# Optimization experiments

Hardware: AMD Instinct MI355X
Metric: run time of the kernel (lower is better)

## Reference

```python
import jax, jax.numpy as jnp
import numpy as np

BATCH, SEQ, D_MODEL = 2, 2048, 1024
NUM_HEADS = 16
D_K = D_MODEL // NUM_HEADS  # 64
ROPE_THETA = 10000.0


def setup_inputs() -> dict:
    key = jax.random.key(0)
    ks = jax.random.split(key, 5)
    sigma = np.sqrt(2.0 / (D_MODEL + D_MODEL))
    return {
        "x": jax.random.normal(ks[0], (BATCH, SEQ, D_MODEL), dtype=jnp.float32),
        "Wq": jax.random.normal(ks[1], (D_MODEL, D_MODEL), dtype=jnp.float32) * sigma,
        "Wk": jax.random.normal(ks[2], (D_MODEL, D_MODEL), dtype=jnp.float32) * sigma,
        "Wv": jax.random.normal(ks[3], (D_MODEL, D_MODEL), dtype=jnp.float32) * sigma,
        "Wo": jax.random.normal(ks[4], (D_MODEL, D_MODEL), dtype=jnp.float32) * sigma,
        "token_positions": jnp.arange(SEQ, dtype=jnp.int32),
    }


def _rope(t, cos, sin):
    # t: [b, h, s, d_k]; cos/sin: [s, d_k//2]
    even, odd = t[..., ::2], t[..., 1::2]
    out_even = even * cos - odd * sin
    out_odd = odd * cos + even * sin
    return jnp.stack([out_even, out_odd], axis=-1).reshape(t.shape)


def reference(x, Wq, Wk, Wv, Wo, token_positions):
    b, s, d = x.shape
    h, dk = NUM_HEADS, D_K

    def split_heads(w):
        # Linear: einsum('... d_in, d_out d_in -> ... d_out')
        y = jnp.einsum('bsd,ed->bse', x, w)
        return y.reshape(b, s, h, dk).transpose(0, 2, 1, 3)  # [b,h,s,dk]

    q, k, v = split_heads(Wq), split_heads(Wk), split_heads(Wv)

    # RoPE tables from token positions
    inv_freq = 1.0 / (ROPE_THETA ** (jnp.arange(0, dk, 2, dtype=jnp.float32) / dk))
    freqs = token_positions.astype(jnp.float32)[:, None] * inv_freq[None, :]  # [s, dk/2]
    cos, sin = jnp.cos(freqs), jnp.sin(freqs)
    q = _rope(q, cos, sin)
    k = _rope(k, cos, sin)

    scale = 1.0 / jnp.sqrt(jnp.asarray(dk, dtype=x.dtype))
    scores = jnp.einsum('bhqd,bhkd->bhqk', q, k) * scale  # [b,h,s,s]
    causal = jnp.tril(jnp.ones((s, s), dtype=bool))
    scores = jnp.where(causal, scores, -jnp.inf)
    probs = jax.nn.softmax(scores, axis=-1)
    out = jnp.einsum('bhqk,bhkd->bhqd', probs, v)
    out = out.transpose(0, 2, 1, 3).reshape(b, s, d)
    return jnp.einsum('bsd,ed->bse', out, Wo)
```

## Files before the change

kernel.cpp:

```cpp
#include <hip/hip_runtime.h>
#include <hip/hip_bf16.h>


#define BATCH   2
#define SEQLEN  2048
#define DMODEL  1024
#define NHEADS  16
#define DK      64

typedef __attribute__((ext_vector_type(8))) short bf16x8;
typedef __attribute__((ext_vector_type(4))) short bf16x4;
typedef __attribute__((ext_vector_type(4))) float f32x4;

__device__ __forceinline__ float fast_exp2(float x) {
#if __has_builtin(__builtin_amdgcn_exp2f)
  return __builtin_amdgcn_exp2f(x);
#else
  return exp2f(x);
#endif
}

__device__ __forceinline__ bf16x8 load_cvt(const __hip_bfloat16* p) {
  return *(const bf16x8*)p;
}
__device__ __forceinline__ bf16x8 load_cvt(const float* p) {
  float4 a = *(const float4*)p;
  float4 b = *(const float4*)(p + 4);
  __hip_bfloat16 t[8];
  t[0] = __float2bfloat16(a.x); t[1] = __float2bfloat16(a.y);
  t[2] = __float2bfloat16(a.z); t[3] = __float2bfloat16(a.w);
  t[4] = __float2bfloat16(b.x); t[5] = __float2bfloat16(b.y);
  t[6] = __float2bfloat16(b.z); t[7] = __float2bfloat16(b.w);
  return *(const bf16x8*)t;
}

template <typename TA, typename TW>
__device__ __forceinline__ void gemm_core(
    const TA* __restrict__ A, const TW* __restrict__ W,
    int bm, int bn, int K, f32x4 (&acc)[4][4]) {
  __shared__ __hip_bfloat16 As[2][128 * 32];
  __shared__ __hip_bfloat16 Ws[2][128 * 32];
  const int tid  = threadIdx.x;
  const int wave = tid >> 6, lane = tid & 63;
  const int col  = lane & 15, quad = lane >> 4;
  const int wm   = (wave & 1) * 64, wn = (wave >> 1) * 64;
  const int srow = wave * 32;
  const int l4   = lane >> 2, sl = lane & 3;

  bf16x8 ra[2], rw[2];
  auto stage_load = [&](int k0) {
#pragma unroll
    for (int c = 0; c < 2; ++c) {
      int r = srow + c * 16 + l4;
      int g = sl ^ (r & 3);
      ra[c] = load_cvt(A + (size_t)(bm + r) * K + k0 + g * 8);
      rw[c] = load_cvt(W + (size_t)(bn + r) * K + k0 + g * 8);
    }
  };
  auto stage_write = [&](int buf) {
#pragma unroll
    for (int c = 0; c < 2; ++c) {
      int r = srow + c * 16 + l4;
      *(bf16x8*)&As[buf][r * 32 + sl * 8] = ra[c];
      *(bf16x8*)&Ws[buf][r * 32 + sl * 8] = rw[c];
    }
  };

  const int NK = K / 32;
  stage_load(0);
  stage_write(0);
  __syncthreads();

  for (int i = 0; i < NK; ++i) {
    const int buf = i & 1;
    const bool pre = (i + 1 < NK);
    if (pre) stage_load((i + 1) * 32);

    bf16x8 af[4], bfr[4];
#pragma unroll
    for (int mt = 0; mt < 4; ++mt) {
      int r = wm + mt * 16 + col;
      af[mt] = *(const bf16x8*)&As[buf][r * 32 + ((quad ^ (r & 3)) * 8)];
    }
#pragma unroll
    for (int nt = 0; nt < 4; ++nt) {
      int r = wn + nt * 16 + col;
      bfr[nt] = *(const bf16x8*)&Ws[buf][r * 32 + ((quad ^ (r & 3)) * 8)];
    }
#pragma unroll
    for (int mt = 0; mt < 4; ++mt)
#pragma unroll
      for (int nt = 0; nt < 4; ++nt)
        acc[mt][nt] = __builtin_amdgcn_mfma_f32_16x16x32_bf16(af[mt], bfr[nt], acc[mt][nt], 0, 0, 0);

    if (pre) stage_write(buf ^ 1);
    __syncthreads();
  }
}

__global__ __launch_bounds__(256) void mfma_qkv(
    const float* __restrict__ x,
    const float* __restrict__ wq,
    const float* __restrict__ wk,
    const float* __restrict__ wv,
    __hip_bfloat16* __restrict__ Qw,
    __hip_bfloat16* __restrict__ Kw,
    __hip_bfloat16* __restrict__ Vtw) {
  const int z = blockIdx.z;
  const float* W = (z == 0) ? wq : (z == 1) ? wk : wv;
  const int bm = blockIdx.x * 128, bn = blockIdx.y * 128;
  f32x4 acc[4][4] = {};
  gemm_core(x, W, bm, bn, DMODEL, acc);

  const int wave = threadIdx.x >> 6, lane = threadIdx.x & 63;
  const int col  = lane & 15, quad = lane >> 4;
  const int wm   = (wave & 1) * 64, wn = (wave >> 1) * 64;

  if (z < 2) {
    __hip_bfloat16* C = (z == 0) ? Qw : Kw;
#pragma unroll
    for (int mt = 0; mt < 4; ++mt)
#pragma unroll
      for (int nt = 0; nt < 4; ++nt) {
        int n = bn + wn + nt * 16 + col;
#pragma unroll
        for (int r = 0; r < 4; ++r) {
          int m = bm + wm + mt * 16 + quad * 4 + r;
          C[(size_t)m * DMODEL + n] = __float2bfloat16(acc[mt][nt][r]);
        }
      }
  } else {
#pragma unroll
    for (int mt = 0; mt < 4; ++mt)
#pragma unroll
      for (int nt = 0; nt < 4; ++nt) {
        int n  = bn + wn + nt * 16 + col;
        int m0 = bm + wm + mt * 16 + quad * 4;
        __hip_bfloat16 t[4];
#pragma unroll
        for (int r = 0; r < 4; ++r) t[r] = __float2bfloat16(acc[mt][nt][r]);
        size_t off = (((size_t)(m0 >> 11) * NHEADS + (n >> 6)) * DK + (n & 63)) * SEQLEN + (m0 & 2047);
        *(bf16x4*)(Vtw + off) = *(const bf16x4*)t;
      }
  }
}

__global__ __launch_bounds__(256) void mfma_out(
    const __hip_bfloat16* __restrict__ Ow,
    const float* __restrict__ wo,
    float* __restrict__ out) {
  const int bm = blockIdx.x * 128, bn = blockIdx.y * 128;
  f32x4 acc[4][4] = {};
  gemm_core(Ow, wo, bm, bn, DMODEL, acc);
  const int wave = threadIdx.x >> 6, lane = threadIdx.x & 63;
  const int col  = lane & 15, quad = lane >> 4;
  const int wm   = (wave & 1) * 64, wn = (wave >> 1) * 64;
#pragma unroll
  for (int mt = 0; mt < 4; ++mt)
#pragma unroll
    for (int nt = 0; nt < 4; ++nt) {
      int n = bn + wn + nt * 16 + col;
#pragma unroll
      for (int r = 0; r < 4; ++r) {
        int m = bm + wm + mt * 16 + quad * 4 + r;
        out[(size_t)m * DMODEL + n] = acc[mt][nt][r];
      }
    }
}

__global__ __launch_bounds__(256) void rope_kernel(
    __hip_bfloat16* __restrict__ Q,
    __hip_bfloat16* __restrict__ Kt,
    const int* __restrict__ pos, int npairs) {
  int idx = blockIdx.x * blockDim.x + threadIdx.x;
  if (idx >= npairs) return;
  int ip = idx & 511;
  int s  = (idx >> 9) & (SEQLEN - 1);
  int p  = ip & 31;
  float inv_freq = exp2f(-13.287712379549449f * ((float)(2 * p) / 64.0f));
  float ang = (float)pos[s] * inv_freq;
  float sn, cs;
  sincosf(ang, &sn, &cs);
  const float SCL = 0.18033688011112042f;
  size_t off = (size_t)idx * 2;
  float qe = __bfloat162float(Q[off]), qo = __bfloat162float(Q[off + 1]);
  Q[off]     = __float2bfloat16((qe * cs - qo * sn) * SCL);
  Q[off + 1] = __float2bfloat16((qo * cs + qe * sn) * SCL);
  float ke = __bfloat162float(Kt[off]), ko = __bfloat162float(Kt[off + 1]);
  Kt[off]     = __float2bfloat16(ke * cs - ko * sn);
  Kt[off + 1] = __float2bfloat16(ko * cs + ke * sn);
}

__global__ __launch_bounds__(512) void attn_mfma(
    const __hip_bfloat16* __restrict__ Q,
    const __hip_bfloat16* __restrict__ K,
    const __hip_bfloat16* __restrict__ Vt,
    __hip_bfloat16* __restrict__ O) {
  __shared__ __align__(16) __hip_bfloat16 Ks[2][64 * 64];
  __shared__ __align__(16) __hip_bfloat16 Vs[2][64 * 64];
  __shared__ __align__(16) __hip_bfloat16 Pl[8][32 * 64];
  const int lin  = (int)blockIdx.y * (int)gridDim.x + (int)blockIdx.x;
  const int xcd  = lin & 7, slot = lin >> 3;
  const int bh   = xcd * 4 + (slot & 3);
  const int strip = 15 - (slot >> 2);
  const int b = bh >> 4, h = bh & 15;
  const int wave = threadIdx.x >> 6;
  const int lane = threadIdx.x & 63;
  const int qg = wave & 3;
  const int kg = wave >> 2;
  const int col = lane & 15, quad = lane >> 4;
  const int q0w = strip * 128 + qg * 32;
  const int cswz = col & 7;

  const size_t qkbase = ((size_t)b * SEQLEN) * DMODEL + (size_t)h * DK;
  const size_t vbase  = (size_t)bh * DK * SEQLEN;
  __hip_bfloat16* pl = &Pl[wave][0];

  const int sr = ((int)threadIdx.x >> 3) & 63;
  const int sl = (int)threadIdx.x & 7;
  const int sgch = sl ^ (sr & 7);

  bf16x8 stK[2], stV[2];
  auto stage_load = [&](int p) {
    const int j0 = p * 128;
#pragma unroll
    for (int g = 0; g < 2; ++g) {
      stK[g] = *(const bf16x8*)(K + qkbase + (size_t)(j0 + g * 64 + sr) * DMODEL + sgch * 8);
      stV[g] = *(const bf16x8*)(Vt + vbase + (size_t)sr * SEQLEN + j0 + g * 64 + sgch * 8);
    }
  };
  auto stage_write = [&]() {
#pragma unroll
    for (int g = 0; g < 2; ++g) {
      *(bf16x8*)&Ks[g][sr * 64 + sl * 8] = stK[g];
      *(bf16x8*)&Vs[g][sr * 64 + sl * 8] = stV[g];
    }
  };

  bf16x8 qf[2][2];
#pragma unroll
  for (int qt = 0; qt < 2; ++qt)
#pragma unroll
    for (int kc = 0; kc < 2; ++kc)
      qf[qt][kc] = *(const bf16x8*)(Q + qkbase +
          (size_t)(q0w + qt * 16 + col) * DMODEL + kc * 32 + quad * 8);

  f32x4 acc[2][4] = {};
  float l_i[2] = {0.f, 0.f};

  const bool skip_last = (kg == 1) && (qg < 2);

  stage_load(0);
  stage_write();
  __syncthreads();

  for (int p = 0; p <= strip; ++p) {
    const bool pre  = p < strip;
    const bool last = p == strip;
    if (pre) stage_load(p + 1);

    if (!(last && skip_last)) {
      const int kb = p * 128 + kg * 64;

      f32x4 s[2][4] = {};
#pragma unroll
      for (int kt = 0; kt < 4; ++kt) {
        const int row = kt * 16 + col;
#pragma unroll
        for (int kc = 0; kc < 2; ++kc) {
          bf16x8 kf = *(const bf16x8*)&Ks[kg][row * 64 + (((kc * 4 + quad) ^ cswz) * 8)];
#pragma unroll
          for (int qt = 0; qt < 2; ++qt)
            s[qt][kt] = __builtin_amdgcn_mfma_f32_16x16x32_bf16(kf, qf[qt][kc], s[qt][kt], 0, 0, 0);
        }
      }

      if (last) {
#pragma unroll
        for (int qt = 0; qt < 2; ++qt) {
          const int q = q0w + qt * 16 + col;
#pragma unroll
          for (int kt = 0; kt < 4; ++kt)
#pragma unroll
            for (int r = 0; r < 4; ++r)
              if (kb + kt * 16 + quad * 4 + r > q) s[qt][kt][r] = -1e30f;
        }
      }

#pragma unroll
      for (int qt = 0; qt < 2; ++qt) {
#pragma unroll
        for (int kt = 0; kt < 4; ++kt) {
          __hip_bfloat16 tp[4];
#pragma unroll
          for (int r = 0; r < 4; ++r) {
            float pv = fast_exp2(s[qt][kt][r] - 24.0f);
            l_i[qt] += pv;
            tp[r] = __float2bfloat16(pv);
          }
          int c2 = ((kt << 1) | (quad >> 1)) ^ cswz;
          *(bf16x4*)(pl + (qt * 16 + col) * 64 + c2 * 8 + (quad & 1) * 4) = *(const bf16x4*)tp;
        }
      }

#pragma unroll
      for (int jc = 0; jc < 2; ++jc) {
        const int c2 = ((jc << 2) | quad) ^ cswz;
        bf16x8 pf[2];
#pragma unroll
        for (int qt = 0; qt < 2; ++qt)
          pf[qt] = *(const bf16x8*)(pl + (qt * 16 + col) * 64 + c2 * 8);
#pragma unroll
        for (int dt = 0; dt < 4; ++dt) {
          const int dv = dt * 16 + col;
          bf16x8 vf = *(const bf16x8*)&Vs[kg][dv * 64 + (((jc * 4 + quad) ^ cswz) * 8)];
#pragma unroll
          for (int qt = 0; qt < 2; ++qt)
            acc[qt][dt] = __builtin_amdgcn_mfma_f32_16x16x32_bf16(vf, pf[qt], acc[qt][dt], 0, 0, 0);
        }
      }
    }

    __syncthreads();
    if (pre) { stage_write(); __syncthreads(); }
  }

  float* accbuf = (float*)&Pl[0][0];
  float* lbuf   = (float*)&Ks[0][0];
  if (kg == 1) {
#pragma unroll
    for (int qt = 0; qt < 2; ++qt)
#pragma unroll
      for (int dt = 0; dt < 4; ++dt)
        *(f32x4*)(accbuf + ((qg * 8 + qt * 4 + dt) * 64 + lane) * 4) = acc[qt][dt];
    lbuf[(qg * 64 + lane) * 2 + 0] = l_i[0];
    lbuf[(qg * 64 + lane) * 2 + 1] = l_i[1];
  }
  __syncthreads();
  if (kg == 0) {
#pragma unroll
    for (int qt = 0; qt < 2; ++qt)
#pragma unroll
      for (int dt = 0; dt < 4; ++dt) {
        f32x4 o = *(const f32x4*)(accbuf + ((qg * 8 + qt * 4 + dt) * 64 + lane) * 4);
        acc[qt][dt] += o;
      }
    l_i[0] += lbuf[(qg * 64 + lane) * 2 + 0];
    l_i[1] += lbuf[(qg * 64 + lane) * 2 + 1];

#pragma unroll
    for (int qt = 0; qt < 2; ++qt) {
      float l = l_i[qt];
      l += __shfl_xor(l, 16, 64);
      l += __shfl_xor(l, 32, 64);
      const float inv = 1.f / l;
      const size_t orow = qkbase + (size_t)(q0w + qt * 16 + col) * DMODEL;
#pragma unroll
      for (int dt = 0; dt < 4; ++dt) {
        __hip_bfloat16 tp[4];
#pragma unroll
        for (int r = 0; r < 4; ++r) tp[r] = __float2bfloat16(acc[qt][dt][r] * inv);
        *(bf16x4*)(O + orow + dt * 16 + quad * 4) = *(const bf16x4*)tp;
      }
    }
  }
}

extern "C" void kernel_launch(void* const* d_in, const int* in_sizes, int n_in,
                              void* d_out, int out_size, void* d_ws, size_t ws_size,
                              hipStream_t stream) {
  const float* x  = (const float*)d_in[0];
  const float* Wq = (const float*)d_in[1];
  const float* Wk = (const float*)d_in[2];
  const float* Wv = (const float*)d_in[3];
  const float* Wo = (const float*)d_in[4];
  const int* pos  = (const int*)d_in[5];
  float* out = (float*)d_out;

  const size_t NELEM = (size_t)BATCH * SEQLEN * DMODEL;
  __hip_bfloat16* Qw  = (__hip_bfloat16*)d_ws;
  __hip_bfloat16* Kw  = Qw + NELEM;
  __hip_bfloat16* Vtw = Kw + NELEM;
  __hip_bfloat16* Ow  = Vtw + NELEM;

  mfma_qkv<<<dim3(32, 8, 3), 256, 0, stream>>>(x, Wq, Wk, Wv, Qw, Kw, Vtw);

  int npairs = BATCH * SEQLEN * (DMODEL / 2);
  rope_kernel<<<(npairs + 255) / 256, 256, 0, stream>>>(Qw, Kw, pos, npairs);

  attn_mfma<<<dim3(16, BATCH * NHEADS), 512, 0, stream>>>(Qw, Kw, Vtw, Ow);

  mfma_out<<<dim3(32, 8), 256, 0, stream>>>(Ow, Wo, out);
}
```

Baseline: 187.5 us.

## Split K across two wave groups in projection GEMMs with LDS reduction

The QKV and output projection GEMMs now launch 512 threads per block. Each group of four waves handles half of the K dimension in its own double-buffered LDS tiles, and the two partial accumulators are summed through shared memory before the epilogue. The aim is more waves per block to hide load and convert latency, since each block previously ran only four waves over a long K loop. The cost is double the LDS footprint (64 KB), an extra reduction pass, and possibly lower occupancy from register pressure at 512 threads.

```diff
diff --git a/kernel.cpp b/kernel.cpp
--- a/kernel.cpp
+++ b/kernel.cpp
@@ -35,17 +35,20 @@
 }
 
 template <typename TA, typename TW>
-__device__ __forceinline__ void gemm_core(
+__device__ __forceinline__ void gemm_core_ks(
     const TA* __restrict__ A, const TW* __restrict__ W,
     int bm, int bn, int K, f32x4 (&acc)[4][4]) {
-  __shared__ __hip_bfloat16 As[2][128 * 32];
-  __shared__ __hip_bfloat16 Ws[2][128 * 32];
+  __shared__ __hip_bfloat16 As[2][2][128 * 32];
+  __shared__ __hip_bfloat16 Ws[2][2][128 * 32];
   const int tid  = threadIdx.x;
   const int wave = tid >> 6, lane = tid & 63;
+  const int kh   = wave >> 2;
+  const int wq   = wave & 3;
   const int col  = lane & 15, quad = lane >> 4;
-  const int wm   = (wave & 1) * 64, wn = (wave >> 1) * 64;
-  const int srow = wave * 32;
+  const int wm   = (wq & 1) * 64, wn = (wq >> 1) * 64;
+  const int srow = wq * 32;
   const int l4   = lane >> 2, sl = lane & 3;
+  const int kbase = kh * (K >> 1);
 
   bf16x8 ra[2], rw[2];
   auto stage_load = [&](int k0) {
@@ -53,20 +56,20 @@
     for (int c = 0; c < 2; ++c) {
       int r = srow + c * 16 + l4;
       int g = sl ^ (r & 3);
-      ra[c] = load_cvt(A + (size_t)(bm + r) * K + k0 + g * 8);
-      rw[c] = load_cvt(W + (size_t)(bn + r) * K + k0 + g * 8);
+      ra[c] = load_cvt(A + (size_t)(bm + r) * K + kbase + k0 + g * 8);
+      rw[c] = load_cvt(W + (size_t)(bn + r) * K + kbase + k0 + g * 8);
     }
   };
   auto stage_write = [&](int buf) {
 #pragma unroll
     for (int c = 0; c < 2; ++c) {
       int r = srow + c * 16 + l4;
-      *(bf16x8*)&As[buf][r * 32 + sl * 8] = ra[c];
-      *(bf16x8*)&Ws[buf][r * 32 + sl * 8] = rw[c];
+      *(bf16x8*)&As[kh][buf][r * 32 + sl * 8] = ra[c];
+      *(bf16x8*)&Ws[kh][buf][r * 32 + sl * 8] = rw[c];
     }
   };
 
-  const int NK = K / 32;
+  const int NK = K >> 6;
   stage_load(0);
   stage_write(0);
   __syncthreads();
@@ -80,12 +83,12 @@
 #pragma unroll
     for (int mt = 0; mt < 4; ++mt) {
       int r = wm + mt * 16 + col;
-      af[mt] = *(const bf16x8*)&As[buf][r * 32 + ((quad ^ (r & 3)) * 8)];
+      af[mt] = *(const bf16x8*)&As[kh][buf][r * 32 + ((quad ^ (r & 3)) * 8)];
     }
 #pragma unroll
     for (int nt = 0; nt < 4; ++nt) {
       int r = wn + nt * 16 + col;
-      bfr[nt] = *(const bf16x8*)&Ws[buf][r * 32 + ((quad ^ (r & 3)) * 8)];
+      bfr[nt] = *(const bf16x8*)&Ws[kh][buf][r * 32 + ((quad ^ (r & 3)) * 8)];
     }
 #pragma unroll
     for (int mt = 0; mt < 4; ++mt)
@@ -96,9 +99,27 @@
     if (pre) stage_write(buf ^ 1);
     __syncthreads();
   }
-}
-
-__global__ __launch_bounds__(256) void mfma_qkv(
+
+  float* red = (wq < 2) ? (float*)&As[0][0][0] : (float*)&Ws[0][0][0];
+  float* reg = red + (wq & 1) * 4096;
+  if (kh == 1) {
+#pragma unroll
+    for (int mt = 0; mt < 4; ++mt)
+#pragma unroll
+      for (int nt = 0; nt < 4; ++nt)
+        *(f32x4*)(reg + ((mt * 4 + nt) * 64 + lane) * 4) = acc[mt][nt];
+  }
+  __syncthreads();
+  if (kh == 0) {
+#pragma unroll
+    for (int mt = 0; mt < 4; ++mt)
+#pragma unroll
+      for (int nt = 0; nt < 4; ++nt)
+        acc[mt][nt] += *(const f32x4*)(reg + ((mt * 4 + nt) * 64 + lane) * 4);
+  }
+}
+
+__global__ __launch_bounds__(512) void mfma_qkv(
     const float* __restrict__ x,
     const float* __restrict__ wq,
     const float* __restrict__ wk,
@@ -110,7 +131,8 @@
   const float* W = (z == 0) ? wq : (z == 1) ? wk : wv;
   const int bm = blockIdx.x * 128, bn = blockIdx.y * 128;
   f32x4 acc[4][4] = {};
-  gemm_core(x, W, bm, bn, DMODEL, acc);
+  gemm_core_ks(x, W, bm, bn, DMODEL, acc);
+  if (threadIdx.x >= 256) return;
 
   const int wave = threadIdx.x >> 6, lane = threadIdx.x & 63;
   const int col  = lane & 15, quad = lane >> 4;
@@ -145,13 +167,15 @@
   }
 }
 
-__global__ __launch_bounds__(256) void mfma_out(
+__global__ __launch_bounds__(512) void mfma_out(
     const __hip_bfloat16* __restrict__ Ow,
     const float* __restrict__ wo,
     float* __restrict__ out) {
   const int bm = blockIdx.x * 128, bn = blockIdx.y * 128;
   f32x4 acc[4][4] = {};
-  gemm_core(Ow, wo, bm, bn, DMODEL, acc);
+  gemm_core_ks(Ow, wo, bm, bn, DMODEL, acc);
+  if (threadIdx.x >= 256) return;
+
   const int wave = threadIdx.x >> 6, lane = threadIdx.x & 63;
   const int col  = lane & 15, quad = lane >> 4;
   const int wm   = (wave & 1) * 64, wn = (wave >> 1) * 64;
@@ -383,12 +407,12 @@
   __hip_bfloat16* Vtw = Kw + NELEM;
   __hip_bfloat16* Ow  = Vtw + NELEM;
 
-  mfma_qkv<<<dim3(32, 8, 3), 256, 0, stream>>>(x, Wq, Wk, Wv, Qw, Kw, Vtw);
+  mfma_qkv<<<dim3(32, 8, 3), 512, 0, stream>>>(x, Wq, Wk, Wv, Qw, Kw, Vtw);
 
   int npairs = BATCH * SEQLEN * (DMODEL / 2);
   rope_kernel<<<(npairs + 255) / 256, 256, 0, stream>>>(Qw, Kw, pos, npairs);
 
   attn_mfma<<<dim3(16, BATCH * NHEADS), 512, 0, stream>>>(Qw, Kw, Vtw, Ow);
 
-  mfma_out<<<dim3(32, 8), 256, 0, stream>>>(Ow, Wo, out);
-}
+  mfma_out<<<dim3(32, 8), 512, 0, stream>>>(Ow, Wo, out);
+}
```

Measured after the change: 209.9 us. 1.12x slower.
